# Kernel tuning notes

Hardware: AMD Instinct MI355X
Metric: run time of the kernel (lower is better)

Reference implementation:

```python
import jax, jax.numpy as jnp
import numpy as np
from jax import lax

BOX_STRIDES = (32, 64, 128, 256)
MASK_STRIDE = 4
MASK_SIZE = 28
PATCH = 512
TOPK = 64
SCORE_TH = 0.5
IOU_TH = 0.5
MASK_TH = 0.5


def setup_inputs():
    key = jax.random.key(0)
    ks = jax.random.split(key, 10)
    d = {}
    d["pred0"] = jax.random.normal(ks[0], (2, 6, 16, 16), jnp.float32)
    d["pred1"] = jax.random.normal(ks[1], (2, 6, 8, 8), jnp.float32)
    d["pred2"] = jax.random.normal(ks[2], (2, 6, 4, 4), jnp.float32)
    d["pred3"] = jax.random.normal(ks[3], (2, 6, 2, 2), jnp.float32)
    d["feat0"] = jax.random.normal(ks[4], (2, 64, 128, 128), jnp.float32)
    d["feat1"] = jax.random.normal(ks[5], (2, 64, 64, 64), jnp.float32)
    d["feat2"] = jax.random.normal(ks[6], (2, 64, 32, 32), jnp.float32)
    d["feat3"] = jax.random.normal(ks[7], (2, 64, 16, 16), jnp.float32)
    d["w1"] = jax.random.normal(ks[8], (128, 256, 3, 3), jnp.float32) * 0.05
    d["b1"] = jnp.zeros((128,), jnp.float32)
    d["w2"] = jax.random.normal(ks[9], (1, 128, 1, 1), jnp.float32) * 0.05
    d["b2"] = jnp.zeros((1,), jnp.float32)
    return d


def _decode_level(pred, stride):
    # pred: [B, 6, H, W] -> [B, H*W, 6], (cx,cy)=(p+grid)*stride, wh=exp(p)*stride
    B, no, H, W = pred.shape
    p = pred.transpose(0, 2, 3, 1).reshape(B, H * W, no)
    gy, gx = jnp.meshgrid(jnp.arange(H), jnp.arange(W), indexing="ij")
    grid = jnp.stack([gx.ravel(), gy.ravel()], axis=-1).astype(p.dtype)  # [HW,2] (x,y)
    xy = (p[..., 0:2] + grid) * stride
    wh = jnp.exp(p[..., 2:4]) * stride
    return jnp.concatenate([xy, wh, p[..., 4:]], axis=-1)


def _iou_matrix(b):
    # b: [K,4] xyxy
    area = jnp.clip(b[:, 2] - b[:, 0], 0) * jnp.clip(b[:, 3] - b[:, 1], 0)
    ix0 = jnp.maximum(b[:, None, 0], b[None, :, 0])
    iy0 = jnp.maximum(b[:, None, 1], b[None, :, 1])
    ix1 = jnp.minimum(b[:, None, 2], b[None, :, 2])
    iy1 = jnp.minimum(b[:, None, 3], b[None, :, 3])
    inter = jnp.clip(ix1 - ix0, 0) * jnp.clip(iy1 - iy0, 0)
    union = area[:, None] + area[None, :] - inter
    return inter / jnp.maximum(union, 1e-9)


def _nms_keep(boxes, labels, valid):
    # boxes already sorted by descending score; batched NMS via per-class coord offset
    off = labels.astype(boxes.dtype)[:, None] * (PATCH * 8.0)
    iou = _iou_matrix(boxes + off)
    idx = jnp.arange(TOPK)

    def body(i, keep):
        sup = keep[i] & (iou[i] > IOU_TH) & (idx > i)
        return keep & ~sup

    return lax.fori_loop(0, TOPK, body, valid)


def _roi_align_one(feat, box):
    # feat: [C,Hf,Wf]; box: [4] xyxy in image coords (spatial_scale=1/MASK_STRIDE)
    # torchvision-style aligned=False, one bilinear sample per bin center
    C, Hf, Wf = feat.shape
    b = box / MASK_STRIDE
    bw = (b[2] - b[0]) / MASK_SIZE
    bh = (b[3] - b[1]) / MASK_SIZE
    xs = b[0] + (jnp.arange(MASK_SIZE, dtype=feat.dtype) + 0.5) * bw
    ys = b[1] + (jnp.arange(MASK_SIZE, dtype=feat.dtype) + 0.5) * bh
    x = jnp.clip(jnp.broadcast_to(xs[None, :], (MASK_SIZE, MASK_SIZE)), 0.0, Wf - 1.0)
    y = jnp.clip(jnp.broadcast_to(ys[:, None], (MASK_SIZE, MASK_SIZE)), 0.0, Hf - 1.0)
    x0 = jnp.floor(x).astype(jnp.int32)
    y0 = jnp.floor(y).astype(jnp.int32)
    x1 = jnp.minimum(x0 + 1, Wf - 1)
    y1 = jnp.minimum(y0 + 1, Hf - 1)
    fx = x - x0
    fy = y - y0
    v00 = feat[:, y0, x0]
    v01 = feat[:, y0, x1]
    v10 = feat[:, y1, x0]
    v11 = feat[:, y1, x1]
    return (v00 * (1 - fy) * (1 - fx) + v01 * (1 - fy) * fx
            + v10 * fy * (1 - fx) + v11 * fy * fx)  # [C,S,S]


def _paste_one(mask_soft, box_int):
    # nearest-neighbor upsample of [S,S] mask into its box on a [P,P] canvas
    x0, y0, x1, y1 = box_int[0], box_int[1], box_int[2], box_int[3]
    h = y1 - y0 + 1
    w = x1 - x0 + 1
    ys = jnp.arange(PATCH, dtype=jnp.int32)
    xs = jnp.arange(PATCH, dtype=jnp.int32)
    iy = jnp.clip((ys - y0) * MASK_SIZE // h, 0, MASK_SIZE - 1)
    ix = jnp.clip((xs - x0) * MASK_SIZE // w, 0, MASK_SIZE - 1)
    g = mask_soft[iy][:, ix]  # [P,P]
    inside = ((ys >= y0) & (ys <= y1))[:, None] & ((xs >= x0) & (xs <= x1))[None, :]
    return jnp.where(inside, g, 0.0)


def _conv(x, w, b, pad):
    y = lax.conv_general_dilated(x, w, (1, 1), pad, dimension_numbers=("NCHW", "OIHW", "NCHW"))
    return y + b[None, :, None, None]


def _pipeline(pred0, pred1, pred2, pred3, feat0, feat1, feat2, feat3, w1, b1, w2, b2):
    # box branch: decode per-level predictions
    yolo = jnp.concatenate(
        [_decode_level(p, s) for p, s in zip([pred0, pred1, pred2, pred3], BOX_STRIDES)],
        axis=1,
    )  # [B,N,6]
    B = yolo.shape[0]
    cx, cy, w_, h_ = yolo[..., 0], yolo[..., 1], yolo[..., 2], yolo[..., 3]
    boxes = jnp.stack([cx - w_ / 2, cy - h_ / 2, cx + w_ / 2, cy + h_ / 2], axis=-1)
    scores = jax.nn.sigmoid(yolo[..., 4])
    labels = jnp.argmax(yolo[..., 5:], axis=-1)
    valid = scores > SCORE_TH
    top_scores, top_idx = lax.top_k(jnp.where(valid, scores, 0.0), TOPK)
    boxes_k = jnp.take_along_axis(boxes, top_idx[..., None], axis=1)  # [B,K,4]
    labels_k = jnp.take_along_axis(labels, top_idx, axis=1)
    valid_k = top_scores > SCORE_TH
    keep = jax.vmap(_nms_keep)(boxes_k, labels_k, valid_k)  # [B,K] bool

    # mask branch: merge mask feats at the first level's resolution (nearest)
    H0, W0 = feat0.shape[2], feat0.shape[3]
    merged = jnp.concatenate(
        [feat0] + [jax.image.resize(f, (B, f.shape[1], H0, W0), "nearest") for f in [feat1, feat2, feat3]],
        axis=1,
    )  # [B,256,H0,W0]
    rois = jax.vmap(lambda f, bx: jax.vmap(lambda bb: _roi_align_one(f, bb))(bx))(merged, boxes_k)
    C = rois.shape[2]
    x = rois.reshape(B * TOPK, C, MASK_SIZE, MASK_SIZE)
    hdn = jax.nn.silu(_conv(x, w1, b1, "SAME"))
    logits = _conv(hdn, w2, b2, "SAME")  # [B*K,1,S,S]
    soft = jax.nn.sigmoid(logits).reshape(B, TOPK, MASK_SIZE, MASK_SIZE)

    box_int = jnp.clip(boxes_k, 0, PATCH - 1).astype(jnp.int32)
    pasted = jax.vmap(jax.vmap(_paste_one))(soft, box_int)  # [B,K,P,P]
    return top_scores, boxes_k, labels_k, pasted, keep


def reference(pred0, pred1, pred2, pred3, feat0, feat1, feat2, feat3, w1, b1, w2, b2):
    top_scores, boxes_k, labels_k, pasted, keep = _pipeline(
        pred0, pred1, pred2, pred3, feat0, feat1, feat2, feat3, w1, b1, w2, b2
    )
    out_scores = top_scores * keep
    bin_masks = (pasted > MASK_TH) & keep[:, :, None, None]
    return out_scores, boxes_k, labels_k.astype(jnp.int32), bin_masks, keep
```

## Files before the change

kernel.cpp:

```cpp
#include <hip/hip_runtime.h>
#include <hip/hip_bf16.h>
#include <cstdint>

#define NTOPK 64
#define A_TOT 340
#define MS 28

#define OFF_SCORES 0
#define OFF_BOXES  128
#define OFF_LABELS 640
#define OFF_MASKS  768
#define OFF_KEEP   33555200ull

typedef __attribute__((ext_vector_type(4))) float f32x4;
typedef long fp8x8;

__device__ __forceinline__ float sigmoidf_(float x) { return 1.f / (1.f + expf(-x)); }
__device__ __forceinline__ float bf2f(unsigned u) {
  return __uint_as_float(u << 16);
}
__device__ __forceinline__ unsigned short f2bf(float f) {
  __hip_bfloat16 h = __float2bfloat16(f);
  return *(unsigned short*)&h;
}

__global__ __launch_bounds__(256) void k_prep(
    const float* __restrict__ p0, const float* __restrict__ p1,
    const float* __restrict__ p2, const float* __restrict__ p3,
    const float* __restrict__ f0, const float* __restrict__ f1,
    const float* __restrict__ f2, const float* __restrict__ f3,
    const float* __restrict__ w1,
    float* __restrict__ out,
    float* __restrict__ ws_boxes, int* __restrict__ ws_keep,
    int* __restrict__ ws_boxint,
    unsigned char* __restrict__ wt, unsigned short* __restrict__ mg)
{
  __shared__ __align__(16) char smem_raw[128 * 260 * 2];
  const int bid = blockIdx.x;
  const int t = threadIdx.x;

  if (bid < 2) {
    const int b = bid;
    float* sc = (float*)smem_raw;
    float(*bx)[4] = (float(*)[4])(sc + A_TOT);
    float* tk_score = (float*)(bx + A_TOT);
    float(*tk_box)[4] = (float(*)[4])(tk_score + 64);

    for (int a = t; a < A_TOT; a += 256) {
      const float* pp; int W, HW, la; float stride;
      if (a < 256)      { pp = p0; W = 16; HW = 256; la = a;       stride = 32.f;  }
      else if (a < 320) { pp = p1; W = 8;  HW = 64;  la = a - 256; stride = 64.f;  }
      else if (a < 336) { pp = p2; W = 4;  HW = 16;  la = a - 320; stride = 128.f; }
      else              { pp = p3; W = 2;  HW = 4;   la = a - 336; stride = 256.f; }
      const float* base = pp + (size_t)b * 6 * HW + la;
      float v0 = base[0], v1 = base[HW], v2 = base[2 * HW], v3 = base[3 * HW], v4 = base[4 * HW];
      int gx = la % W, gy = la / W;
      float cx = (v0 + (float)gx) * stride;
      float cy = (v1 + (float)gy) * stride;
      float w_ = expf(v2) * stride;
      float h_ = expf(v3) * stride;
      float score = sigmoidf_(v4);
      sc[a] = (score > 0.5f) ? score : 0.f;
      bx[a][0] = cx - 0.5f * w_;
      bx[a][1] = cy - 0.5f * h_;
      bx[a][2] = cx + 0.5f * w_;
      bx[a][3] = cy + 0.5f * h_;
    }
    __syncthreads();

    for (int a = t; a < A_TOT; a += 256) {
      float my = sc[a];
      int rank = 0;
      for (int j = 0; j < A_TOT; ++j) {
        float o = sc[j];
        rank += (o > my) || (o == my && j < a);
      }
      if (rank < NTOPK) {
        tk_score[rank] = my;
        tk_box[rank][0] = bx[a][0];
        tk_box[rank][1] = bx[a][1];
        tk_box[rank][2] = bx[a][2];
        tk_box[rank][3] = bx[a][3];
      }
    }
    __syncthreads();

    if (t < NTOPK) {
      float x0 = tk_box[t][0], y0 = tk_box[t][1];
      float x1 = tk_box[t][2], y1 = tk_box[t][3];
      float s = tk_score[t];
      float area = fmaxf(x1 - x0, 0.f) * fmaxf(y1 - y0, 0.f);
      int keep = (s > 0.5f) ? 1 : 0;
      for (int i = 0; i < NTOPK - 1; ++i) {
        int   ki = __shfl(keep, i);
        float a0 = __shfl(x0, i);
        float c0 = __shfl(y0, i);
        float a1 = __shfl(x1, i);
        float c1 = __shfl(y1, i);
        float ai = __shfl(area, i);
        if (ki && t > i && keep) {
          float ix0 = fmaxf(a0, x0), iy0 = fmaxf(c0, y0);
          float ix1 = fminf(a1, x1), iy1 = fminf(c1, y1);
          float inter = fmaxf(ix1 - ix0, 0.f) * fmaxf(iy1 - iy0, 0.f);
          float uni = ai + area - inter;
          float iou = inter / fmaxf(uni, 1e-9f);
          if (iou > 0.5f) keep = 0;
        }
      }
      int box = b * NTOPK + t;
      out[OFF_SCORES + box] = keep ? s : 0.f;
      float bv[4] = {x0, y0, x1, y1};
      #pragma unroll
      for (int c = 0; c < 4; ++c) {
        out[OFF_BOXES + box * 4 + c] = bv[c];
        ws_boxes[box * 4 + c] = bv[c];
        float bc = fminf(fmaxf(bv[c], 0.f), 511.f);
        ws_boxint[box * 4 + c] = (int)bc;
      }
      out[OFF_LABELS + box] = 0.f;
      out[OFF_KEEP + box] = keep ? 1.f : 0.f;
      ws_keep[box] = keep;
    }
    return;
  }

  if (bid < 130) {
    const int co = bid - 2;
    const int ci = t;
    const int c = ci >> 5, cil = ci & 31;
    const int cq = co >> 5, col = co & 31;
    const int slot = ((cil >> 3) ^ ((col >> 2) & 3)) * 8 + (cil & 7);
    const float* src = w1 + ((size_t)co * 256 + ci) * 9;
    #pragma unroll
    for (int tap = 0; tap < 9; ++tap) {
      unsigned u = __builtin_amdgcn_cvt_pk_fp8_f32(src[tap], 0.f, 0, false);
      wt[(((size_t)(c * 4 + cq) * 9 + tap)) * 1024 + col * 32 + slot] =
          (unsigned char)(u & 0xff);
    }
    return;
  }

  {
    const int idx = bid - 130;
    const int b = idx >> 7;
    const int y = idx & 127;
    unsigned short* tile = (unsigned short*)smem_raw;
    const int x = t & 127, ch = t >> 7;

    {
      const float* src = f0 + ((size_t)b * 64) * 16384 + y * 128 + x;
      for (int cc = 0; cc < 32; ++cc) {
        int cl = ch * 32 + cc;
        tile[x * 260 + cl] = f2bf(src[(size_t)cl * 16384]);
      }
    }
    {
      const float* src = f1 + ((size_t)b * 64) * 4096 + (y >> 1) * 64 + (x >> 1);
      for (int cc = 0; cc < 32; ++cc) {
        int cl = ch * 32 + cc;
        tile[x * 260 + 64 + cl] = f2bf(src[(size_t)cl * 4096]);
      }
    }
    {
      const float* src = f2 + ((size_t)b * 64) * 1024 + (y >> 2) * 32 + (x >> 2);
      for (int cc = 0; cc < 32; ++cc) {
        int cl = ch * 32 + cc;
        tile[x * 260 + 128 + cl] = f2bf(src[(size_t)cl * 1024]);
      }
    }
    {
      const float* src = f3 + ((size_t)b * 64) * 256 + (y >> 3) * 16 + (x >> 3);
      for (int cc = 0; cc < 32; ++cc) {
        int cl = ch * 32 + cc;
        tile[x * 260 + 192 + cl] = f2bf(src[(size_t)cl * 256]);
      }
    }
    __syncthreads();
    unsigned short* dst = mg + (((size_t)b * 128 + y) * 128) * 256;
    for (int it = 0; it < 32; ++it) {
      int qq = t + it * 256;
      int xx = qq >> 6, cg = qq & 63;
      *(ushort4*)(dst + xx * 256 + cg * 4) = *(ushort4*)&tile[xx * 260 + cg * 4];
    }
  }
}

__global__ __launch_bounds__(256) void k_roistage(
    const unsigned short* __restrict__ mg,
    const float* __restrict__ ws_boxes, const int* __restrict__ ws_keep,
    unsigned char* __restrict__ roi)
{
  const int boxLo = blockIdx.x & 7;
  const int r2 = blockIdx.x >> 3;
  const int r = r2 % 30;
  const int box = ((r2 / 30) << 3) | boxLo;
  if (!ws_keep[box]) return;
  const int t = threadIdx.x;
  unsigned char* rbox = roi + (size_t)box * 8 * 30 * 1024;
  const int gr = r - 1;

  if (gr < 0 || gr > 27) {
    uint2 z = {0u, 0u};
    for (int e = t; e < 1024; e += 256) {
      int chunk = e >> 7, rem = e & 127;
      int cell = rem >> 2, quad = rem & 3;
      size_t off = ((size_t)(chunk * 30 + r)) * 1024 + cell * 32 +
                   (quad ^ ((cell >> 2) & 3)) * 8;
      *(uint2*)(rbox + off) = z;
    }
    return;
  }

  __shared__ int   xa_s[MS], xb_s[MS];
  __shared__ float fx_s[MS];
  __shared__ float by_s[4];
  if (t < 4) by_s[t] = ws_boxes[box * 4 + t];
  __syncthreads();
  const float b0 = by_s[0] * 0.25f, b1_ = by_s[1] * 0.25f;
  const float b2_ = by_s[2] * 0.25f, b3_ = by_s[3] * 0.25f;
  if (t < MS) {
    float bw = (b2_ - b0) * (1.f / MS);
    float x = b0 + ((float)t + 0.5f) * bw;
    x = fminf(fmaxf(x, 0.f), 127.f);
    int x0 = (int)floorf(x);
    xa_s[t] = x0; xb_s[t] = min(x0 + 1, 127); fx_s[t] = x - (float)x0;
  }
  float bh = (b3_ - b1_) * (1.f / MS);
  float yy = b1_ + ((float)gr + 0.5f) * bh;
  yy = fminf(fmaxf(yy, 0.f), 127.f);
  int ya = (int)floorf(yy);
  int yb = min(ya + 1, 127);
  float fy = yy - (float)ya;
  __syncthreads();

  const int b = box >> 6;
  const unsigned short* mgb = mg + ((size_t)b * 128 * 128) * 256;

  for (int e = t; e < 1024; e += 256) {
    int chunk = e >> 7, rem = e & 127;
    int cell = rem >> 2, quad = rem & 3;
    size_t off = ((size_t)(chunk * 30 + r)) * 1024 + cell * 32 +
                 (quad ^ ((cell >> 2) & 3)) * 8;
    int gc = cell - 1;
    if (gc < 0 || gc > 27) {
      uint2 z = {0u, 0u};
      *(uint2*)(rbox + off) = z;
      continue;
    }
    int U = chunk * 4 + quad;
    int xa = xa_s[gc], xb = xb_s[gc];
    float fx = fx_s[gc];
    float w00 = (1.f - fy) * (1.f - fx), w01 = (1.f - fy) * fx;
    float w10 = fy * (1.f - fx),         w11 = fy * fx;
    uint4 A = *(const uint4*)(mgb + ((size_t)(ya * 128 + xa)) * 256 + U * 8);
    uint4 B = *(const uint4*)(mgb + ((size_t)(ya * 128 + xb)) * 256 + U * 8);
    uint4 C = *(const uint4*)(mgb + ((size_t)(yb * 128 + xa)) * 256 + U * 8);
    uint4 D = *(const uint4*)(mgb + ((size_t)(yb * 128 + xb)) * 256 + U * 8);
    const unsigned* pa = (const unsigned*)&A;
    const unsigned* pb = (const unsigned*)&B;
    const unsigned* pc = (const unsigned*)&C;
    const unsigned* pd = (const unsigned*)&D;
    float f[8];
    #pragma unroll
    for (int k2 = 0; k2 < 4; ++k2) {
      f[2 * k2] = bf2f(pa[k2] & 0xffffu) * w00 + bf2f(pb[k2] & 0xffffu) * w01 +
                  bf2f(pc[k2] & 0xffffu) * w10 + bf2f(pd[k2] & 0xffffu) * w11;
      f[2 * k2 + 1] = bf2f(pa[k2] >> 16) * w00 + bf2f(pb[k2] >> 16) * w01 +
                      bf2f(pc[k2] >> 16) * w10 + bf2f(pd[k2] >> 16) * w11;
    }
    unsigned o0 = __builtin_amdgcn_cvt_pk_fp8_f32(f[0], f[1], 0, false);
    o0 = __builtin_amdgcn_cvt_pk_fp8_f32(f[2], f[3], o0, true);
    unsigned o1 = __builtin_amdgcn_cvt_pk_fp8_f32(f[4], f[5], 0, false);
    o1 = __builtin_amdgcn_cvt_pk_fp8_f32(f[6], f[7], o1, true);
    uint2 pk; pk.x = o0; pk.y = o1;
    *(uint2*)(rbox + off) = pk;
  }
}

__global__ __launch_bounds__(512, 4) void k_conv(
    const unsigned char* __restrict__ roi,
    const unsigned char* __restrict__ wt,
    const float* __restrict__ b1, const float* __restrict__ w2,
    const int* __restrict__ ws_keep,
    float* __restrict__ ws_logit4)
{
  const int bid = blockIdx.x;
  const int boxLo = bid & 7;
  const int r1 = bid >> 3;
  const int q = r1 & 3;
  const int box = ((r1 >> 2) << 3) | boxLo;
  if (!ws_keep[box]) return;
  const int t = threadIdx.x;
  const int lane = t & 63, wv = t >> 6;
  const int cq = wv >> 1, half = wv & 1;
  const int laneN = lane & 15, kg = lane >> 4;

  __shared__ __align__(16) unsigned char lds[46080];

  int badd[7][3];
  bool act[7];
  #pragma unroll
  for (int i = 0; i < 7; ++i) {
    int tile = half * 7 + i;
    act[i] = tile < 13;
    int p = tile * 16 + laneN;
    if (p > 195) p = 195;
    int py = p / 28, px = p - py * 28;
    #pragma unroll
    for (int dx = 0; dx < 3; ++dx) {
      int cell = px + dx;
      badd[i][dx] = 36864 + py * 1024 + cell * 32 + (kg ^ ((cell >> 2) & 3)) * 8;
    }
  }
  const int aswz = (kg ^ ((laneN >> 2) & 3)) * 8;

  f32x4 acc[2][7];
  #pragma unroll
  for (int m = 0; m < 2; ++m)
    #pragma unroll
    for (int i = 0; i < 7; ++i) acc[m][i] = (f32x4){0.f, 0.f, 0.f, 0.f};

  const uint4* rbase = (const uint4*)roi;
  const uint4* wbase = (const uint4*)wt;

  uint4 ga0, ga1, ga2, ga3, ga4;
  uint4 gb0, gb1;
  auto issue_load = [&](int c) {
    const uint4* wa = wbase + (size_t)c * 2304;
    ga0 = wa[t]; ga1 = wa[t + 512]; ga2 = wa[t + 1024]; ga3 = wa[t + 1536];
    if (t < 256) ga4 = wa[t + 2048];
    const uint4* s = rbase + ((size_t)(box * 8 + c) * 30 + q * 7) * 64;
    gb0 = s[t];
    if (t < 64) gb1 = s[t + 512];
  };
  auto write_lds = [&]() {
    uint4* da = (uint4*)lds;
    da[t] = ga0; da[t + 512] = ga1; da[t + 1024] = ga2; da[t + 1536] = ga3;
    if (t < 256) da[t + 2048] = ga4;
    uint4* db = (uint4*)(lds + 36864);
    db[t] = gb0;
    if (t < 64) db[t + 512] = gb1;
  };

  issue_load(0);
  const unsigned char* la = lds + (size_t)cq * 9216;

  #pragma unroll 1
  for (int c = 0; c < 8; ++c) {
    write_lds();
    __syncthreads();
    if (c < 7) issue_load(c + 1);
    #pragma unroll
    for (int tap = 0; tap < 9; ++tap) {
      const int dy = tap / 3, dx = tap - dy * 3;
      fp8x8 av0 = *(const fp8x8*)(la + tap * 1024 + laneN * 32 + aswz);
      fp8x8 av1 = *(const fp8x8*)(la + tap * 1024 + 512 + laneN * 32 + aswz);
      #pragma unroll
      for (int i = 0; i < 7; ++i) {
        if (act[i]) {
          fp8x8 bv = *(const fp8x8*)(lds + badd[i][dx] + dy * 1024);
          acc[0][i] = __builtin_amdgcn_mfma_f32_16x16x32_fp8_fp8(av0, bv, acc[0][i], 0, 0, 0);
          acc[1][i] = __builtin_amdgcn_mfma_f32_16x16x32_fp8_fp8(av1, bv, acc[1][i], 0, 0, 0);
        }
      }
    }
    __syncthreads();
  }

  float b1v[2][4], w2v[2][4];
  #pragma unroll
  for (int m = 0; m < 2; ++m)
    #pragma unroll
    for (int r = 0; r < 4; ++r) {
      int co = cq * 32 + m * 16 + kg * 4 + r;
      b1v[m][r] = b1[co];
      w2v[m][r] = w2[co];
    }
  #pragma unroll
  for (int i = 0; i < 7; ++i) {
    if (!act[i]) continue;
    float part = 0.f;
    #pragma unroll
    for (int m = 0; m < 2; ++m)
      #pragma unroll
      for (int r = 0; r < 4; ++r) {
        float h = acc[m][i][r] + b1v[m][r];
        part = fmaf(w2v[m][r], h * sigmoidf_(h), part);
      }
    part += __shfl_xor(part, 16);
    part += __shfl_xor(part, 32);
    int p = (half * 7 + i) * 16 + laneN;
    if (kg == 0 && p < 196)
      ws_logit4[((size_t)box * 4 + cq) * 784 + q * 196 + p] = part;
  }
}

__global__ __launch_bounds__(256) void k_paste(
    const float* __restrict__ ws_logit4, const int* __restrict__ ws_keep,
    const int* __restrict__ ws_boxint, const float* __restrict__ b2,
    float* __restrict__ out)
{
  const int box = blockIdx.x >> 4;
  const int yo  = blockIdx.x & 15;
  const int t = threadIdx.x;
  float* mb = out + OFF_MASKS + (size_t)box * 262144 + (size_t)yo * 32 * 512;

  if (!ws_keep[box]) {
    f32x4 z = {0.f, 0.f, 0.f, 0.f};
    f32x4* p = (f32x4*)mb;
    for (int e = t; e < 4096; e += 256)
      __builtin_nontemporal_store(z, p + e);
    return;
  }

  __shared__ float soft[784];
  __shared__ int iys[32];
  __shared__ int bi[4];
  if (t < 4) bi[t] = ws_boxint[box * 4 + t];
  __syncthreads();
  const int x0 = bi[0], y0 = bi[1], x1 = bi[2], y1 = bi[3];
  const int w = x1 - x0 + 1, h = y1 - y0 + 1;
  const float b2v = b2[0];
  const float* l0 = ws_logit4 + (size_t)box * 4 * 784;

  for (int e = t; e < 784; e += 256)
    soft[e] = sigmoidf_(l0[e] + l0[784 + e] + l0[1568 + e] + l0[2352 + e] + b2v);
  if (t < 32) {
    int Y = yo * 32 + t;
    int vy = (Y - y0) * MS;
    int iy = (vy >= 0) ? (vy / h) : 0;
    iys[t] = min(max(iy, 0), MS - 1);
  }
  __syncthreads();

  const int c4 = (t & 127) * 4;
  const int rr = t >> 7;
  int ixr[4];
  bool inx[4];
  #pragma unroll
  for (int u = 0; u < 4; ++u) {
    int X = c4 + u;
    int vx = (X - x0) * MS;
    int ix = (vx >= 0) ? (vx / w) : 0;
    ixr[u] = min(max(ix, 0), MS - 1);
    inx[u] = (X >= x0) && (X <= x1);
  }

  int prev_iy = -1;
  f32x4 v = {0.f, 0.f, 0.f, 0.f};
  #pragma unroll 1
  for (int it = 0; it < 16; ++it) {
    int Yl = it * 2 + rr;
    int Y = yo * 32 + Yl;
    f32x4 o;
    if (Y >= y0 && Y <= y1) {
      int iy = iys[Yl];
      if (iy != prev_iy) {
        prev_iy = iy;
        #pragma unroll
        for (int u = 0; u < 4; ++u)
          v[u] = (inx[u] && soft[iy * MS + ixr[u]] > 0.5f) ? 1.f : 0.f;
      }
      o = v;
    } else {
      o = (f32x4){0.f, 0.f, 0.f, 0.f};
    }
    __builtin_nontemporal_store(o, (f32x4*)(mb + (size_t)Yl * 512 + c4));
  }
}

extern "C" void kernel_launch(void* const* d_in, const int* in_sizes, int n_in,
                              void* d_out, int out_size, void* d_ws, size_t ws_size,
                              hipStream_t stream) {
  const float* p0 = (const float*)d_in[0];
  const float* p1 = (const float*)d_in[1];
  const float* p2 = (const float*)d_in[2];
  const float* p3 = (const float*)d_in[3];
  const float* f0 = (const float*)d_in[4];
  const float* f1 = (const float*)d_in[5];
  const float* f2 = (const float*)d_in[6];
  const float* f3 = (const float*)d_in[7];
  const float* w1 = (const float*)d_in[8];
  const float* b1 = (const float*)d_in[9];
  const float* w2 = (const float*)d_in[10];
  const float* b2 = (const float*)d_in[11];
  float* out = (float*)d_out;

  float* wsf = (float*)d_ws;
  float*          ws_boxes  = wsf;
  int*            ws_keep   = (int*)(wsf + 512);
  int*            ws_boxint = (int*)(wsf + 640);
  float*          ws_logit4 = wsf + 1152;
  unsigned char*  ws_wt     = (unsigned char*)(wsf + 402560);
  unsigned short* ws_merged = (unsigned short*)(wsf + 476288);
  unsigned char*  ws_roi    = (unsigned char*)(wsf + 4670592);

  k_prep<<<386, 256, 0, stream>>>(p0, p1, p2, p3, f0, f1, f2, f3, w1,
                                  out, ws_boxes, ws_keep, ws_boxint,
                                  ws_wt, ws_merged);
  k_roistage<<<3840, 256, 0, stream>>>(ws_merged, ws_boxes, ws_keep, ws_roi);
  k_conv<<<512, 512, 0, stream>>>(ws_roi, ws_wt, b1, w2, ws_keep, ws_logit4);
  k_paste<<<2048, 256, 0, stream>>>(ws_logit4, ws_keep, ws_boxint, b2, out);
}
```

Before: 263.2 us.

## Fuse ROI-align and mask paste into the conv kernel

Merges the ROI-align stage into the conv kernel: each block builds its 9-row bilinear-sampled fp8 input slice straight into LDS for every channel chunk, so the ROI workspace round-trip is gone. The conv epilogue now reduces the four channel-quarter partials in shared memory, applies the sigmoid, and pastes its own band of output rows, which also removes the logit workspace and the separate paste kernel. This cuts two kernel launches and the global traffic between them. In exchange the conv loop's critical path now includes the gather of four bilinear taps, and paste parallelism drops from 2048 blocks to 512.

```diff
diff --git a/kernel.cpp b/kernel.cpp
--- a/kernel.cpp
+++ b/kernel.cpp
@@ -13,6 +13,7 @@
 #define OFF_KEEP   33555200ull
 
 typedef __attribute__((ext_vector_type(4))) float f32x4;
+typedef __attribute__((ext_vector_type(2))) float f32x2;
 typedef long fp8x8;
 
 __device__ __forceinline__ float sigmoidf_(float x) { return 1.f / (1.f + expf(-x)); }
@@ -185,117 +186,71 @@
   }
 }
 
-__global__ __launch_bounds__(256) void k_roistage(
+__global__ __launch_bounds__(512, 4) void k_conv(
     const unsigned short* __restrict__ mg,
-    const float* __restrict__ ws_boxes, const int* __restrict__ ws_keep,
-    unsigned char* __restrict__ roi)
-{
-  const int boxLo = blockIdx.x & 7;
-  const int r2 = blockIdx.x >> 3;
-  const int r = r2 % 30;
-  const int box = ((r2 / 30) << 3) | boxLo;
-  if (!ws_keep[box]) return;
-  const int t = threadIdx.x;
-  unsigned char* rbox = roi + (size_t)box * 8 * 30 * 1024;
-  const int gr = r - 1;
-
-  if (gr < 0 || gr > 27) {
-    uint2 z = {0u, 0u};
-    for (int e = t; e < 1024; e += 256) {
-      int chunk = e >> 7, rem = e & 127;
-      int cell = rem >> 2, quad = rem & 3;
-      size_t off = ((size_t)(chunk * 30 + r)) * 1024 + cell * 32 +
-                   (quad ^ ((cell >> 2) & 3)) * 8;
-      *(uint2*)(rbox + off) = z;
-    }
-    return;
-  }
-
-  __shared__ int   xa_s[MS], xb_s[MS];
-  __shared__ float fx_s[MS];
-  __shared__ float by_s[4];
-  if (t < 4) by_s[t] = ws_boxes[box * 4 + t];
-  __syncthreads();
-  const float b0 = by_s[0] * 0.25f, b1_ = by_s[1] * 0.25f;
-  const float b2_ = by_s[2] * 0.25f, b3_ = by_s[3] * 0.25f;
-  if (t < MS) {
-    float bw = (b2_ - b0) * (1.f / MS);
-    float x = b0 + ((float)t + 0.5f) * bw;
-    x = fminf(fmaxf(x, 0.f), 127.f);
-    int x0 = (int)floorf(x);
-    xa_s[t] = x0; xb_s[t] = min(x0 + 1, 127); fx_s[t] = x - (float)x0;
-  }
-  float bh = (b3_ - b1_) * (1.f / MS);
-  float yy = b1_ + ((float)gr + 0.5f) * bh;
-  yy = fminf(fmaxf(yy, 0.f), 127.f);
-  int ya = (int)floorf(yy);
-  int yb = min(ya + 1, 127);
-  float fy = yy - (float)ya;
-  __syncthreads();
-
-  const int b = box >> 6;
-  const unsigned short* mgb = mg + ((size_t)b * 128 * 128) * 256;
-
-  for (int e = t; e < 1024; e += 256) {
-    int chunk = e >> 7, rem = e & 127;
-    int cell = rem >> 2, quad = rem & 3;
-    size_t off = ((size_t)(chunk * 30 + r)) * 1024 + cell * 32 +
-                 (quad ^ ((cell >> 2) & 3)) * 8;
-    int gc = cell - 1;
-    if (gc < 0 || gc > 27) {
-      uint2 z = {0u, 0u};
-      *(uint2*)(rbox + off) = z;
-      continue;
-    }
-    int U = chunk * 4 + quad;
-    int xa = xa_s[gc], xb = xb_s[gc];
-    float fx = fx_s[gc];
-    float w00 = (1.f - fy) * (1.f - fx), w01 = (1.f - fy) * fx;
-    float w10 = fy * (1.f - fx),         w11 = fy * fx;
-    uint4 A = *(const uint4*)(mgb + ((size_t)(ya * 128 + xa)) * 256 + U * 8);
-    uint4 B = *(const uint4*)(mgb + ((size_t)(ya * 128 + xb)) * 256 + U * 8);
-    uint4 C = *(const uint4*)(mgb + ((size_t)(yb * 128 + xa)) * 256 + U * 8);
-    uint4 D = *(const uint4*)(mgb + ((size_t)(yb * 128 + xb)) * 256 + U * 8);
-    const unsigned* pa = (const unsigned*)&A;
-    const unsigned* pb = (const unsigned*)&B;
-    const unsigned* pc = (const unsigned*)&C;
-    const unsigned* pd = (const unsigned*)&D;
-    float f[8];
-    #pragma unroll
-    for (int k2 = 0; k2 < 4; ++k2) {
-      f[2 * k2] = bf2f(pa[k2] & 0xffffu) * w00 + bf2f(pb[k2] & 0xffffu) * w01 +
-                  bf2f(pc[k2] & 0xffffu) * w10 + bf2f(pd[k2] & 0xffffu) * w11;
-      f[2 * k2 + 1] = bf2f(pa[k2] >> 16) * w00 + bf2f(pb[k2] >> 16) * w01 +
-                      bf2f(pc[k2] >> 16) * w10 + bf2f(pd[k2] >> 16) * w11;
-    }
-    unsigned o0 = __builtin_amdgcn_cvt_pk_fp8_f32(f[0], f[1], 0, false);
-    o0 = __builtin_amdgcn_cvt_pk_fp8_f32(f[2], f[3], o0, true);
-    unsigned o1 = __builtin_amdgcn_cvt_pk_fp8_f32(f[4], f[5], 0, false);
-    o1 = __builtin_amdgcn_cvt_pk_fp8_f32(f[6], f[7], o1, true);
-    uint2 pk; pk.x = o0; pk.y = o1;
-    *(uint2*)(rbox + off) = pk;
-  }
-}
-
-__global__ __launch_bounds__(512, 4) void k_conv(
-    const unsigned char* __restrict__ roi,
     const unsigned char* __restrict__ wt,
     const float* __restrict__ b1, const float* __restrict__ w2,
-    const int* __restrict__ ws_keep,
-    float* __restrict__ ws_logit4)
+    const float* __restrict__ b2,
+    const float* __restrict__ ws_boxes, const int* __restrict__ ws_keep,
+    const int* __restrict__ ws_boxint,
+    float* __restrict__ out)
 {
   const int bid = blockIdx.x;
   const int boxLo = bid & 7;
   const int r1 = bid >> 3;
   const int q = r1 & 3;
   const int box = ((r1 >> 2) << 3) | boxLo;
-  if (!ws_keep[box]) return;
   const int t = threadIdx.x;
+
+  float* mb = out + OFF_MASKS + (size_t)box * 262144;
+
+  if (!ws_keep[box]) {
+    f32x4 z = {0.f, 0.f, 0.f, 0.f};
+    f32x4* p = (f32x4*)(mb + (size_t)q * 128 * 512);
+    for (int e = t; e < 16384; e += 512)
+      __builtin_nontemporal_store(z, p + e);
+    return;
+  }
+
   const int lane = t & 63, wv = t >> 6;
   const int cq = wv >> 1, half = wv & 1;
   const int laneN = lane & 15, kg = lane >> 4;
 
   __shared__ __align__(16) unsigned char lds[46080];
+  __shared__ float psum[4][200];
+  __shared__ float softm[7][28];
+  __shared__ int   xa_s[MS], xb_s[MS];
+  __shared__ float fx_s[MS];
+  __shared__ int   ya_s[9], yb_s[9];
+  __shared__ float fy_s[9];
+  __shared__ float byf[4];
+  __shared__ int   bii[4];
+
+  if (t < 4) { byf[t] = ws_boxes[box * 4 + t]; bii[t] = ws_boxint[box * 4 + t]; }
+  __syncthreads();
+  {
+    const float b0 = byf[0] * 0.25f, b1_ = byf[1] * 0.25f;
+    const float b2_ = byf[2] * 0.25f, b3_ = byf[3] * 0.25f;
+    if (t < MS) {
+      float bw = (b2_ - b0) * (1.f / MS);
+      float x = b0 + ((float)t + 0.5f) * bw;
+      x = fminf(fmaxf(x, 0.f), 127.f);
+      int x0 = (int)floorf(x);
+      xa_s[t] = x0; xb_s[t] = min(x0 + 1, 127); fx_s[t] = x - (float)x0;
+    }
+    if (t < 9) {
+      int gr = q * 7 + t - 1;
+      if (gr < 0 || gr > 27) {
+        ya_s[t] = -1; yb_s[t] = 0; fy_s[t] = 0.f;
+      } else {
+        float bh = (b3_ - b1_) * (1.f / MS);
+        float yy = b1_ + ((float)gr + 0.5f) * bh;
+        yy = fminf(fmaxf(yy, 0.f), 127.f);
+        int ya = (int)floorf(yy);
+        ya_s[t] = ya; yb_s[t] = min(ya + 1, 127); fy_s[t] = yy - (float)ya;
+      }
+    }
+  }
 
   int badd[7][3];
   bool act[7];
@@ -320,36 +275,73 @@
     #pragma unroll
     for (int i = 0; i < 7; ++i) acc[m][i] = (f32x4){0.f, 0.f, 0.f, 0.f};
 
-  const uint4* rbase = (const uint4*)roi;
   const uint4* wbase = (const uint4*)wt;
+  const unsigned short* mgb = mg + ((size_t)(box >> 6) * 128 * 128) * 256;
 
   uint4 ga0, ga1, ga2, ga3, ga4;
-  uint4 gb0, gb1;
-  auto issue_load = [&](int c) {
+  auto issueA = [&](int c) {
     const uint4* wa = wbase + (size_t)c * 2304;
     ga0 = wa[t]; ga1 = wa[t + 512]; ga2 = wa[t + 1024]; ga3 = wa[t + 1536];
     if (t < 256) ga4 = wa[t + 2048];
-    const uint4* s = rbase + ((size_t)(box * 8 + c) * 30 + q * 7) * 64;
-    gb0 = s[t];
-    if (t < 64) gb1 = s[t + 512];
   };
-  auto write_lds = [&]() {
+  auto writeA = [&]() {
     uint4* da = (uint4*)lds;
     da[t] = ga0; da[t + 512] = ga1; da[t + 1024] = ga2; da[t + 1536] = ga3;
     if (t < 256) da[t + 2048] = ga4;
-    uint4* db = (uint4*)(lds + 36864);
-    db[t] = gb0;
-    if (t < 64) db[t + 512] = gb1;
   };
 
-  issue_load(0);
+  issueA(0);
   const unsigned char* la = lds + (size_t)cq * 9216;
+  __syncthreads();
 
   #pragma unroll 1
   for (int c = 0; c < 8; ++c) {
-    write_lds();
+    writeA();
+    #pragma unroll 1
+    for (int e = t; e < 1152; e += 512) {
+      int r = e >> 7, rem = e & 127;
+      int cell = rem >> 2, quad = rem & 3;
+      unsigned char* dst = lds + 36864 + r * 1024 + cell * 32 +
+                           (quad ^ ((cell >> 2) & 3)) * 8;
+      int gc = cell - 1;
+      int ya = ya_s[r];
+      if (gc < 0 || gc > 27 || ya < 0) {
+        uint2 z = {0u, 0u};
+        *(uint2*)dst = z;
+        continue;
+      }
+      int yb = yb_s[r];
+      float fy = fy_s[r];
+      int U = c * 4 + quad;
+      int xa = xa_s[gc], xb = xb_s[gc];
+      float fx = fx_s[gc];
+      float w00 = (1.f - fy) * (1.f - fx), w01 = (1.f - fy) * fx;
+      float w10 = fy * (1.f - fx),         w11 = fy * fx;
+      uint4 A = *(const uint4*)(mgb + ((size_t)(ya * 128 + xa)) * 256 + U * 8);
+      uint4 B = *(const uint4*)(mgb + ((size_t)(ya * 128 + xb)) * 256 + U * 8);
+      uint4 C = *(const uint4*)(mgb + ((size_t)(yb * 128 + xa)) * 256 + U * 8);
+      uint4 D = *(const uint4*)(mgb + ((size_t)(yb * 128 + xb)) * 256 + U * 8);
+      const unsigned* pa = (const unsigned*)&A;
+      const unsigned* pb = (const unsigned*)&B;
+      const unsigned* pc = (const unsigned*)&C;
+      const unsigned* pd = (const unsigned*)&D;
+      float f[8];
+      #pragma unroll
+      for (int k2 = 0; k2 < 4; ++k2) {
+        f[2 * k2] = bf2f(pa[k2] & 0xffffu) * w00 + bf2f(pb[k2] & 0xffffu) * w01 +
+                    bf2f(pc[k2] & 0xffffu) * w10 + bf2f(pd[k2] & 0xffffu) * w11;
+        f[2 * k2 + 1] = bf2f(pa[k2] >> 16) * w00 + bf2f(pb[k2] >> 16) * w01 +
+                        bf2f(pc[k2] >> 16) * w10 + bf2f(pd[k2] >> 16) * w11;
+      }
+      unsigned o0 = __builtin_amdgcn_cvt_pk_fp8_f32(f[0], f[1], 0, false);
+      o0 = __builtin_amdgcn_cvt_pk_fp8_f32(f[2], f[3], o0, true);
+      unsigned o1 = __builtin_amdgcn_cvt_pk_fp8_f32(f[4], f[5], 0, false);
+      o1 = __builtin_amdgcn_cvt_pk_fp8_f32(f[6], f[7], o1, true);
+      uint2 pk; pk.x = o0; pk.y = o1;
+      *(uint2*)dst = pk;
+    }
     __syncthreads();
-    if (c < 7) issue_load(c + 1);
+    if (c < 7) issueA(c + 1);
     #pragma unroll
     for (int tap = 0; tap < 9; ++tap) {
       const int dy = tap / 3, dx = tap - dy * 3;
@@ -367,105 +359,75 @@
     __syncthreads();
   }
 
-  float b1v[2][4], w2v[2][4];
-  #pragma unroll
-  for (int m = 0; m < 2; ++m)
-    #pragma unroll
-    for (int r = 0; r < 4; ++r) {
-      int co = cq * 32 + m * 16 + kg * 4 + r;
-      b1v[m][r] = b1[co];
-      w2v[m][r] = w2[co];
-    }
-  #pragma unroll
-  for (int i = 0; i < 7; ++i) {
-    if (!act[i]) continue;
-    float part = 0.f;
+  {
+    float b1v[2][4], w2v[2][4];
     #pragma unroll
     for (int m = 0; m < 2; ++m)
       #pragma unroll
       for (int r = 0; r < 4; ++r) {
-        float h = acc[m][i][r] + b1v[m][r];
-        part = fmaf(w2v[m][r], h * sigmoidf_(h), part);
-      }
-    part += __shfl_xor(part, 16);
-    part += __shfl_xor(part, 32);
-    int p = (half * 7 + i) * 16 + laneN;
-    if (kg == 0 && p < 196)
-      ws_logit4[((size_t)box * 4 + cq) * 784 + q * 196 + p] = part;
-  }
-}
-
-__global__ __launch_bounds__(256) void k_paste(
-    const float* __restrict__ ws_logit4, const int* __restrict__ ws_keep,
-    const int* __restrict__ ws_boxint, const float* __restrict__ b2,
-    float* __restrict__ out)
-{
-  const int box = blockIdx.x >> 4;
-  const int yo  = blockIdx.x & 15;
-  const int t = threadIdx.x;
-  float* mb = out + OFF_MASKS + (size_t)box * 262144 + (size_t)yo * 32 * 512;
-
-  if (!ws_keep[box]) {
-    f32x4 z = {0.f, 0.f, 0.f, 0.f};
-    f32x4* p = (f32x4*)mb;
-    for (int e = t; e < 4096; e += 256)
-      __builtin_nontemporal_store(z, p + e);
-    return;
-  }
-
-  __shared__ float soft[784];
-  __shared__ int iys[32];
-  __shared__ int bi[4];
-  if (t < 4) bi[t] = ws_boxint[box * 4 + t];
+        int co = cq * 32 + m * 16 + kg * 4 + r;
+        b1v[m][r] = b1[co];
+        w2v[m][r] = w2[co];
+      }
+    #pragma unroll
+    for (int i = 0; i < 7; ++i) {
+      if (!act[i]) continue;
+      float part = 0.f;
+      #pragma unroll
+      for (int m = 0; m < 2; ++m)
+        #pragma unroll
+        for (int r = 0; r < 4; ++r) {
+          float h = acc[m][i][r] + b1v[m][r];
+          part = fmaf(w2v[m][r], h * sigmoidf_(h), part);
+        }
+      part += __shfl_xor(part, 16);
+      part += __shfl_xor(part, 32);
+      int p = (half * 7 + i) * 16 + laneN;
+      if (kg == 0 && p < 196)
+        psum[cq][p] = part;
+    }
+  }
   __syncthreads();
-  const int x0 = bi[0], y0 = bi[1], x1 = bi[2], y1 = bi[3];
-  const int w = x1 - x0 + 1, h = y1 - y0 + 1;
-  const float b2v = b2[0];
-  const float* l0 = ws_logit4 + (size_t)box * 4 * 784;
-
-  for (int e = t; e < 784; e += 256)
-    soft[e] = sigmoidf_(l0[e] + l0[784 + e] + l0[1568 + e] + l0[2352 + e] + b2v);
-  if (t < 32) {
-    int Y = yo * 32 + t;
-    int vy = (Y - y0) * MS;
-    int iy = (vy >= 0) ? (vy / h) : 0;
-    iys[t] = min(max(iy, 0), MS - 1);
+
+  if (t < 196) {
+    float s = sigmoidf_(psum[0][t] + psum[1][t] + psum[2][t] + psum[3][t] + b2[0]);
+    softm[t / 28][t % 28] = s;
   }
   __syncthreads();
 
-  const int c4 = (t & 127) * 4;
-  const int rr = t >> 7;
-  int ixr[4];
-  bool inx[4];
-  #pragma unroll
-  for (int u = 0; u < 4; ++u) {
-    int X = c4 + u;
-    int vx = (X - x0) * MS;
-    int ix = (vx >= 0) ? (vx / w) : 0;
-    ixr[u] = min(max(ix, 0), MS - 1);
-    inx[u] = (X >= x0) && (X <= x1);
-  }
-
-  int prev_iy = -1;
-  f32x4 v = {0.f, 0.f, 0.f, 0.f};
-  #pragma unroll 1
-  for (int it = 0; it < 16; ++it) {
-    int Yl = it * 2 + rr;
-    int Y = yo * 32 + Yl;
-    f32x4 o;
-    if (Y >= y0 && Y <= y1) {
-      int iy = iys[Yl];
-      if (iy != prev_iy) {
-        prev_iy = iy;
-        #pragma unroll
-        for (int u = 0; u < 4; ++u)
-          v[u] = (inx[u] && soft[iy * MS + ixr[u]] > 0.5f) ? 1.f : 0.f;
-      }
-      o = v;
-    } else {
-      o = (f32x4){0.f, 0.f, 0.f, 0.f};
-    }
-    __builtin_nontemporal_store(o, (f32x4*)(mb + (size_t)Yl * 512 + c4));
+  {
+    const int x0 = bii[0], y0 = bii[1], x1 = bii[2], y1 = bii[3];
+    const int w = x1 - x0 + 1, h = y1 - y0 + 1;
+    int Ylo = (q == 0) ? 0 : (y0 + (q * 7 * h + 27) / 28);
+    int Yhi = (q == 3) ? 512 : (y0 + ((q + 1) * 7 * h + 27) / 28);
+    Ylo = min(max(Ylo, 0), 512);
+    Yhi = min(max(Yhi, Ylo), 512);
+
+    const int c4 = (t & 255) * 2;
+    const int rr = t >> 8;
+    int ixr[2];
+    bool inx[2];
+    #pragma unroll
+    for (int u = 0; u < 2; ++u) {
+      int X = c4 + u;
+      int vx = (X - x0) * MS;
+      int ix = (vx >= 0) ? (vx / w) : 0;
+      ixr[u] = min(max(ix, 0), MS - 1);
+      inx[u] = (X >= x0) && (X <= x1);
+    }
+
+    #pragma unroll 1
+    for (int Y = Ylo + rr; Y < Yhi; Y += 2) {
+      f32x2 o = {0.f, 0.f};
+      if (Y >= y0 && Y <= y1) {
+        int vy = (Y - y0) * MS;
+        int iy = min(vy / h, MS - 1);
+        const float* srow = &softm[iy - q * 7][0];
+        o.x = (inx[0] && srow[ixr[0]] > 0.5f) ? 1.f : 0.f;
+        o.y = (inx[1] && srow[ixr[1]] > 0.5f) ? 1.f : 0.f;
+      }
+      __builtin_nontemporal_store(o, (f32x2*)(mb + (size_t)Y * 512 + c4));
+    }
   }
 }
 
@@ -490,15 +452,12 @@
   float*          ws_boxes  = wsf;
   int*            ws_keep   = (int*)(wsf + 512);
   int*            ws_boxint = (int*)(wsf + 640);
-  float*          ws_logit4 = wsf + 1152;
   unsigned char*  ws_wt     = (unsigned char*)(wsf + 402560);
   unsigned short* ws_merged = (unsigned short*)(wsf + 476288);
-  unsigned char*  ws_roi    = (unsigned char*)(wsf + 4670592);
 
   k_prep<<<386, 256, 0, stream>>>(p0, p1, p2, p3, f0, f1, f2, f3, w1,
                                   out, ws_boxes, ws_keep, ws_boxint,
                                   ws_wt, ws_merged);
-  k_roistage<<<3840, 256, 0, stream>>>(ws_merged, ws_boxes, ws_keep, ws_roi);
-  k_conv<<<512, 512, 0, stream>>>(ws_roi, ws_wt, b1, w2, ws_keep, ws_logit4);
-  k_paste<<<2048, 256, 0, stream>>>(ws_logit4, ws_keep, ws_boxint, b2, out);
+  k_conv<<<512, 512, 0, stream>>>(ws_merged, ws_wt, b1, w2, b2,
+                                  ws_boxes, ws_keep, ws_boxint, out);
 }
```

Result: faster. 256.2 us (-2.7%).
